# Kernel tuning notes

Hardware: AMD Instinct MI355X
Metric: run time of the kernel (lower is better)

## Reference

```python
import jax, jax.numpy as jnp
import numpy as np

N_NODES = 50000
N_EDGES = 800000
IN_FEATS = 64
H_FEATS = 128


def _uniform(key, shape, stdv):
    return jax.random.uniform(key, shape, jnp.float32, -stdv, stdv)


def setup_inputs() -> dict:
    key = jax.random.key(0)
    ks = jax.random.split(key, 16)
    inp = {}
    inp["features"] = jax.random.normal(ks[0], (N_NODES, IN_FEATS), jnp.float32)
    inp["mask"] = (jax.random.uniform(ks[1], (N_NODES, IN_FEATS)) > 0.3).astype(jnp.float32)
    inp["norm_g"] = jax.random.uniform(ks[2], (N_NODES, 1), jnp.float32, 0.05, 1.0)
    inp["norm_f"] = jax.random.uniform(ks[3], (N_NODES, 1), jnp.float32, 0.05, 1.0)
    inp["src_g"] = jax.random.randint(ks[4], (N_EDGES,), 0, N_NODES, jnp.int32)
    inp["dst_g"] = jax.random.randint(ks[5], (N_EDGES,), 0, N_NODES, jnp.int32)
    inp["src_f"] = jax.random.randint(ks[6], (N_EDGES,), 0, N_NODES, jnp.int32)
    inp["dst_f"] = jax.random.randint(ks[7], (N_EDGES,), 0, N_NODES, jnp.int32)
    # learned params, init per reset_parameters (uniform +/- 1/sqrt(out_feats))
    s1 = 1.0 / np.sqrt(H_FEATS)
    inp["W1"] = _uniform(ks[8], (IN_FEATS, H_FEATS), s1)
    inp["b1"] = _uniform(ks[9], (H_FEATS,), s1)
    s2 = 1.0 / np.sqrt(IN_FEATS)
    inp["wh"] = _uniform(ks[10], (H_FEATS, IN_FEATS), s2)
    inp["bh"] = _uniform(ks[11], (IN_FEATS,), s2)
    inp["ws"] = _uniform(ks[12], (IN_FEATS, IN_FEATS), s2)
    inp["bs"] = _uniform(ks[13], (IN_FEATS,), s2)
    return inp


def _aggregate(h, src, dst):
    # DGL update_all(copy_src, sum): gather source node feats per edge, sum at dst
    return jax.ops.segment_sum(h[src], dst, num_segments=N_NODES)


def reference(features, mask, norm_g, norm_f, src_g, dst_g, src_f, dst_f,
              W1, b1, wh, bh, ws, bs):
    x = features * mask                     # [N, in]
    # GCL (masked_gcn)
    h = (x @ W1) * norm_g                   # [N, h]
    h = _aggregate(h, src_g, dst_g) * norm_g + b1
    h = jax.nn.relu(h)
    # GCL_skip (output_gcn): h branch on g, skip branch s on f
    hb = (h @ wh) * norm_g                  # [N, in]
    sb = (x @ ws) * norm_f                  # [N, in]
    hb = _aggregate(hb, src_g, dst_g) * norm_g + bh
    sb = _aggregate(sb, src_f, dst_f) * norm_f + bs
    return jax.nn.sigmoid(hb + sb)
```

## Files before the change

kernel.cpp:

```cpp
#include <hip/hip_runtime.h>
#include <hip/hip_fp16.h>

#define N_NODES 50000
#define N_EDGES 800000
#define IN_F 64
#define H_F 128
#define NBUK 49
#define EPB 2048
#define NBLK 391

typedef unsigned short u16;
typedef unsigned int u32;

static __device__ __forceinline__ float4 ld4(const float* p) {
    return *reinterpret_cast<const float4*>(p);
}
static __device__ __forceinline__ void st4(float* p, float4 v) {
    *reinterpret_cast<float4*>(p) = v;
}
static __device__ __forceinline__ void st_h4(__half* p, float4 v) {
    union { __half h[4]; uint2 u; } pk;
    pk.h[0] = __float2half_rn(v.x);
    pk.h[1] = __float2half_rn(v.y);
    pk.h[2] = __float2half_rn(v.z);
    pk.h[3] = __float2half_rn(v.w);
    *reinterpret_cast<uint2*>(p) = pk.u;
}
static __device__ __forceinline__ void add_h4(float4& a, uint2 r) {
    __half2* p = reinterpret_cast<__half2*>(&r);
    float2 f0 = __half22float2(p[0]);
    float2 f1 = __half22float2(p[1]);
    a.x += f0.x; a.y += f0.y; a.z += f1.x; a.w += f1.y;
}

__global__ __launch_bounds__(256) void p1_count_k(
    const int* __restrict__ dst_g, const int* __restrict__ dst_f,
    int* __restrict__ cnt_g, int* __restrict__ cnt_f,
    const float* __restrict__ f, const float* __restrict__ m,
    const float* __restrict__ ng, __half* __restrict__ y)
{
    __shared__ int c[NBUK];
    const int tid = threadIdx.x;
    const int graph = blockIdx.x >= NBLK;
    const int blk = blockIdx.x - graph * NBLK;
    const int* dst = graph ? dst_f : dst_g;
    int* cnt = graph ? cnt_f : cnt_g;
    if (tid < NBUK) c[tid] = 0;
    __syncthreads();
    const int e0 = blk * EPB;
    const int e1 = min(e0 + EPB, N_EDGES);
    for (int e = e0 + tid; e < e1; e += 256) atomicAdd(&c[dst[e] >> 10], 1);
    __syncthreads();
    if (tid < NBUK) cnt[tid * NBLK + blk] = c[tid];
    for (int i = blockIdx.x * 256 + tid; i < N_NODES * (IN_F / 4);
         i += gridDim.x * 256) {
        int n = i >> 4;
        float s = ng[n];
        float4 a = ld4(f + 4 * i);
        float4 b = ld4(m + 4 * i);
        float4 r;
        r.x = a.x * b.x * s; r.y = a.y * b.y * s;
        r.z = a.z * b.z * s; r.w = a.w * b.w * s;
        st_h4(y + 4 * i, r);
    }
}

__global__ __launch_bounds__(1024) void s1_scan_k(
    const int* __restrict__ cnt_g, int* __restrict__ off_g, int* __restrict__ bb_g,
    const int* __restrict__ cnt_f, int* __restrict__ off_f, int* __restrict__ bb_f)
{
    __shared__ int part[1024];
    const int tid = threadIdx.x;
    const int TOT = NBUK * NBLK;
    const int chunk = (TOT + 1023) / 1024;
    for (int g = 0; g < 2; ++g) {
        const int* cnt = g ? cnt_f : cnt_g;
        int* off = g ? off_f : off_g;
        int* bb  = g ? bb_f  : bb_g;
        const int lo = tid * chunk;
        const int hi = min(lo + chunk, TOT);
        int s = 0;
        for (int i = lo; i < hi; ++i) s += cnt[i];
        part[tid] = s;
        __syncthreads();
        for (int o = 1; o < 1024; o <<= 1) {
            int v = (tid >= o) ? part[tid - o] : 0;
            __syncthreads();
            part[tid] += v;
            __syncthreads();
        }
        int ex = (tid == 0) ? 0 : part[tid - 1];
        for (int i = lo; i < hi; ++i) {
            off[i] = ex;
            if (i % NBLK == 0) bb[i / NBLK] = ex;
            ex += cnt[i];
        }
        if (tid == 0) bb[NBUK] = N_EDGES;
        __syncthreads();
    }
}

__global__ __launch_bounds__(256) void p2_part_k(
    const int* __restrict__ src_g, const int* __restrict__ dst_g,
    const int* __restrict__ off_g, u32* __restrict__ rec_g,
    const int* __restrict__ src_f, const int* __restrict__ dst_f,
    const int* __restrict__ off_f, u32* __restrict__ rec_f)
{
    __shared__ int base[NBUK];
    __shared__ int cur[NBUK];
    const int tid = threadIdx.x;
    const int graph = blockIdx.x >= NBLK;
    const int blk = blockIdx.x - graph * NBLK;
    const int* src = graph ? src_f : src_g;
    const int* dst = graph ? dst_f : dst_g;
    const int* off = graph ? off_f : off_g;
    u32* rec = graph ? rec_f : rec_g;
    if (tid < NBUK) { base[tid] = off[tid * NBLK + blk]; cur[tid] = 0; }
    __syncthreads();
    const int e0 = blk * EPB;
    const int e1 = min(e0 + EPB, N_EDGES);
    for (int e = e0 + tid; e < e1; e += 256) {
        int d = dst[e], s = src[e];
        int b = d >> 10;
        int p = atomicAdd(&cur[b], 1);
        rec[base[b] + p] = ((u32)s << 16) | (u32)d;
    }
}

__global__ __launch_bounds__(1024) void p3_build_k(
    const u32* __restrict__ rec_g, const int* __restrict__ bb_g,
    int* __restrict__ rp_g, u16* __restrict__ adj_g,
    const u32* __restrict__ rec_f, const int* __restrict__ bb_f,
    int* __restrict__ rp_f, u16* __restrict__ adj_f)
{
    __shared__ int hist[1024];
    __shared__ int tmp[1024];
    const int tid = threadIdx.x;
    const int graph = blockIdx.x >= NBUK;
    const int b = blockIdx.x - graph * NBUK;
    const u32* rec = graph ? rec_f : rec_g;
    const int* bb  = graph ? bb_f  : bb_g;
    int* rp  = graph ? rp_f : rp_g;
    u16* adj = graph ? adj_f : adj_g;
    const int e_base = bb[b];
    const int e_cnt  = bb[b + 1] - e_base;
    hist[tid] = 0;
    __syncthreads();
    for (int i = tid; i < e_cnt; i += 1024)
        atomicAdd(&hist[rec[e_base + i] & 1023], 1);
    __syncthreads();
    const int v = hist[tid];
    tmp[tid] = v;
    __syncthreads();
    for (int o = 1; o < 1024; o <<= 1) {
        int t = (tid >= o) ? tmp[tid - o] : 0;
        __syncthreads();
        tmp[tid] += t;
        __syncthreads();
    }
    const int excl = tmp[tid] - v;
    const int n = (b << 10) + tid;
    if (n < N_NODES) rp[n] = e_base + excl;
    if (b == NBUK - 1 && tid == 0) rp[N_NODES] = N_EDGES;
    hist[tid] = excl;
    __syncthreads();
    for (int i = tid; i < e_cnt; i += 1024) {
        u32 r = rec[e_base + i];
        int p = atomicAdd(&hist[r & 1023], 1);
        adj[e_base + p] = (u16)(r >> 16);
    }
}

static __device__ __forceinline__ float4 csr_row_sum_h4(
        const __half* __restrict__ tbl, const u16* __restrict__ adj,
        int e, int e1, int off) {
    float4 acc = make_float4(0.f, 0.f, 0.f, 0.f);
    for (; e + 4 <= e1; e += 4) {
        int s0 = adj[e], s1 = adj[e + 1], s2 = adj[e + 2], s3 = adj[e + 3];
        uint2 r0 = *reinterpret_cast<const uint2*>(tbl + (s0 << 6) + off);
        uint2 r1 = *reinterpret_cast<const uint2*>(tbl + (s1 << 6) + off);
        uint2 r2 = *reinterpret_cast<const uint2*>(tbl + (s2 << 6) + off);
        uint2 r3 = *reinterpret_cast<const uint2*>(tbl + (s3 << 6) + off);
        add_h4(acc, r0); add_h4(acc, r1); add_h4(acc, r2); add_h4(acc, r3);
    }
    for (; e < e1; ++e) {
        uint2 r = *reinterpret_cast<const uint2*>(tbl + (adj[e] << 6) + off);
        add_h4(acc, r);
    }
    return acc;
}

__global__ __launch_bounds__(256) void agg64_k(const __half* __restrict__ tbl,
        const int* __restrict__ rp, const u16* __restrict__ adj,
        float* __restrict__ out) {
    const int tid = threadIdx.x;
    const int fl = tid & 15;
    const int n  = blockIdx.x * 16 + (tid >> 4);
    if (n >= N_NODES) return;
    float4 acc = csr_row_sum_h4(tbl, adj, rp[n], rp[n + 1], fl << 2);
    st4(out + (n << 6) + (fl << 2), acc);
}

template<int K, int N, int SMODE, int EPI, int OUT16>
__global__ __launch_bounds__(256) void gemm_k(
    const float* __restrict__ A, const float* __restrict__ A2,
    const float* __restrict__ W, const float* __restrict__ rs,
    const float* __restrict__ bias, void* __restrict__ outv, int M)
{
    constexpr int CPT = N / 16;
    constexpr int AS  = K + 1;
    constexpr int KQ  = K / 4;
    __shared__ __align__(16) float Wl[K * N];
    __shared__ __align__(16) float Al[64 * AS];

    const int tid = threadIdx.x;
    const int n0  = blockIdx.x << 6;

    for (int i = tid; i < K * N / 4; i += 256) st4(&Wl[4 * i], ld4(W + 4 * i));
    for (int i4 = tid; i4 < 64 * KQ; i4 += 256) {
        int n  = i4 / KQ;
        int k4 = (i4 & (KQ - 1)) << 2;
        int gn = n0 + n;
        float4 v = make_float4(0.f, 0.f, 0.f, 0.f);
        if (gn < M) {
            v = ld4(A + gn * K + k4);
            if (SMODE == 1) {
                float4 m4 = ld4(A2 + gn * K + k4);
                v.x *= m4.x; v.y *= m4.y; v.z *= m4.z; v.w *= m4.w;
            }
        }
        float* p = &Al[n * AS + k4];
        p[0] = v.x; p[1] = v.y; p[2] = v.z; p[3] = v.w;
    }
    __syncthreads();

    const int tr = tid & 15;
    const int tc = tid >> 4;

    float acc[4][CPT];
#pragma unroll
    for (int i = 0; i < 4; ++i)
#pragma unroll
        for (int j = 0; j < CPT; ++j) acc[i][j] = 0.f;

#pragma unroll 4
    for (int k = 0; k < K; ++k) {
        float a0 = Al[(4 * tr + 0) * AS + k];
        float a1 = Al[(4 * tr + 1) * AS + k];
        float a2 = Al[(4 * tr + 2) * AS + k];
        float a3 = Al[(4 * tr + 3) * AS + k];
#pragma unroll
        for (int jq = 0; jq < CPT / 4; ++jq) {
            float4 w = ld4(&Wl[k * N + tc * CPT + 4 * jq]);
            acc[0][4 * jq + 0] += a0 * w.x; acc[0][4 * jq + 1] += a0 * w.y;
            acc[0][4 * jq + 2] += a0 * w.z; acc[0][4 * jq + 3] += a0 * w.w;
            acc[1][4 * jq + 0] += a1 * w.x; acc[1][4 * jq + 1] += a1 * w.y;
            acc[1][4 * jq + 2] += a1 * w.z; acc[1][4 * jq + 3] += a1 * w.w;
            acc[2][4 * jq + 0] += a2 * w.x; acc[2][4 * jq + 1] += a2 * w.y;
            acc[2][4 * jq + 2] += a2 * w.z; acc[2][4 * jq + 3] += a2 * w.w;
            acc[3][4 * jq + 0] += a3 * w.x; acc[3][4 * jq + 1] += a3 * w.y;
            acc[3][4 * jq + 2] += a3 * w.z; acc[3][4 * jq + 3] += a3 * w.w;
        }
    }

#pragma unroll
    for (int i = 0; i < 4; ++i) {
        int gn = n0 + 4 * tr + i;
        if (gn >= M) continue;
        float s = rs[gn];
#pragma unroll
        for (int jq = 0; jq < CPT / 4; ++jq) {
            float4 o;
            if (EPI == 1) {
                float4 b4 = ld4(bias + tc * CPT + 4 * jq);
                o.x = fmaxf(fmaf(acc[i][4 * jq + 0], s, b4.x), 0.f);
                o.y = fmaxf(fmaf(acc[i][4 * jq + 1], s, b4.y), 0.f);
                o.z = fmaxf(fmaf(acc[i][4 * jq + 2], s, b4.z), 0.f);
                o.w = fmaxf(fmaf(acc[i][4 * jq + 3], s, b4.w), 0.f);
            } else {
                o.x = acc[i][4 * jq + 0] * s; o.y = acc[i][4 * jq + 1] * s;
                o.z = acc[i][4 * jq + 2] * s; o.w = acc[i][4 * jq + 3] * s;
            }
            if (OUT16) {
                st_h4((__half*)outv + gn * N + tc * CPT + 4 * jq, o);
            } else {
                st4((float*)outv + gn * N + tc * CPT + 4 * jq, o);
            }
        }
    }
}

__global__ __launch_bounds__(256) void final2_k(
    const __half* __restrict__ hb, const __half* __restrict__ sb,
    const int* __restrict__ rp_g, const u16* __restrict__ adj_g,
    const int* __restrict__ rp_f, const u16* __restrict__ adj_f,
    const float* __restrict__ ng, const float* __restrict__ nf,
    const float* __restrict__ bh, const float* __restrict__ bs,
    float* __restrict__ out)
{
    const int tid = threadIdx.x;
    const int fl = tid & 15;
    const int n  = blockIdx.x * 16 + (tid >> 4);
    if (n >= N_NODES) return;
    const int off = fl << 2;
    float4 accg = csr_row_sum_h4(hb, adj_g, rp_g[n], rp_g[n + 1], off);
    float4 accf = csr_row_sum_h4(sb, adj_f, rp_f[n], rp_f[n + 1], off);
    const float g = ng[n], f = nf[n];
    float4 b4 = ld4(bh + off);
    float4 s4 = ld4(bs + off);
    float4 o;
    float t;
    t = accg.x * g + b4.x + accf.x * f + s4.x; o.x = 1.f / (1.f + expf(-t));
    t = accg.y * g + b4.y + accf.y * f + s4.y; o.y = 1.f / (1.f + expf(-t));
    t = accg.z * g + b4.z + accf.z * f + s4.z; o.z = 1.f / (1.f + expf(-t));
    t = accg.w * g + b4.w + accf.w * f + s4.w; o.w = 1.f / (1.f + expf(-t));
    st4(out + (n << 6) + off, o);
}

extern "C" void kernel_launch(void* const* d_in, const int* in_sizes, int n_in,
                              void* d_out, int out_size, void* d_ws, size_t ws_size,
                              hipStream_t stream) {
    const float* features = (const float*)d_in[0];
    const float* mask     = (const float*)d_in[1];
    const float* norm_g   = (const float*)d_in[2];
    const float* norm_f   = (const float*)d_in[3];
    const int*   src_g    = (const int*)d_in[4];
    const int*   dst_g    = (const int*)d_in[5];
    const int*   src_f    = (const int*)d_in[6];
    const int*   dst_f    = (const int*)d_in[7];
    const float* W1  = (const float*)d_in[8];
    const float* b1  = (const float*)d_in[9];
    const float* wh  = (const float*)d_in[10];
    const float* bh  = (const float*)d_in[11];
    const float* wsw = (const float*)d_in[12];
    const float* bs  = (const float*)d_in[13];
    float* out = (float*)d_out;
    float* ws  = (float*)d_ws;

    __half* y   = (__half*)ws;
    float*  z   = ws + 3200000;
    float*  t1  = ws + 6400000;
    __half* hb0 = (__half*)ws;
    __half* sb0 = (__half*)(ws + 3200000);
    int* creg  = (int*)(ws + 6400000);
    u32* rec_g = (u32*)creg;
    u32* rec_f = (u32*)(creg + 800000);
    int* cnt_g = creg + 1600000;
    int* cnt_f = creg + 1619159;
    int* off_g = creg + 1638318;
    int* off_f = creg + 1657477;
    int* pers  = (int*)(ws + 12800000);
    int* rp_g  = pers;
    int* rp_f  = pers + 50001;
    int* bb_g  = pers + 100002;
    int* bb_f  = pers + 100052;
    u16* adj_g = (u16*)(pers + 100102);
    u16* adj_f = (u16*)(pers + 500102);

    const int gblocks = (N_NODES + 63) / 64;
    const int nblk16  = (N_NODES + 15) / 16;

    p1_count_k<<<2 * NBLK, 256, 0, stream>>>(dst_g, dst_f, cnt_g, cnt_f,
                                             features, mask, norm_g, y);
    s1_scan_k<<<1, 1024, 0, stream>>>(cnt_g, off_g, bb_g, cnt_f, off_f, bb_f);
    p2_part_k<<<2 * NBLK, 256, 0, stream>>>(src_g, dst_g, off_g, rec_g,
                                            src_f, dst_f, off_f, rec_f);
    p3_build_k<<<2 * NBUK, 1024, 0, stream>>>(rec_g, bb_g, rp_g, adj_g,
                                              rec_f, bb_f, rp_f, adj_f);

    agg64_k<<<nblk16, 256, 0, stream>>>(y, rp_g, adj_g, z);

    gemm_k<64, 128, 0, 1, 0><<<gblocks, 256, 0, stream>>>(z, nullptr, W1, norm_g,
                                                          b1, (void*)t1, N_NODES);
    gemm_k<128, 64, 0, 2, 1><<<gblocks, 256, 0, stream>>>(t1, nullptr, wh, norm_g,
                                                          nullptr, (void*)hb0, N_NODES);
    gemm_k<64, 64, 1, 2, 1><<<gblocks, 256, 0, stream>>>(features, mask, wsw, norm_f,
                                                         nullptr, (void*)sb0, N_NODES);

    final2_k<<<nblk16, 256, 0, stream>>>(hb0, sb0, rp_g, adj_g, rp_f, adj_f,
                                         norm_g, norm_f, bh, bs, out);
}
```

Before: 294.2 us.

## Build CSR with fixed-capacity buckets via global atomics and widen gather loads

Merges the count, scan and partition passes into one kernel. Each block reserves space in fixed-capacity per-bucket regions through global atomic counters, so the single-block scan kernel and a second pass over the edges go away. Row starts and ends are now stored separately because buckets are no longer contiguous. The aggregation kernels switch to 8 lanes per node with 16-byte half-precision loads in place of 16 lanes with 8-byte loads. The risk is that edges are silently dropped if a bucket ever exceeds its capacity, which assumes a roughly uniform destination distribution.

```diff
diff --git a/kernel.cpp b/kernel.cpp
--- a/kernel.cpp
+++ b/kernel.cpp
@@ -8,6 +8,7 @@
 #define NBUK 49
 #define EPB 2048
 #define NBLK 391
+#define CAP 24576
 
 typedef unsigned short u16;
 typedef unsigned int u32;
@@ -26,32 +27,63 @@
     pk.h[3] = __float2half_rn(v.w);
     *reinterpret_cast<uint2*>(p) = pk.u;
 }
-static __device__ __forceinline__ void add_h4(float4& a, uint2 r) {
+static __device__ __forceinline__ void add_h8(float4& a, float4& b, uint4 r) {
     __half2* p = reinterpret_cast<__half2*>(&r);
     float2 f0 = __half22float2(p[0]);
     float2 f1 = __half22float2(p[1]);
+    float2 f2 = __half22float2(p[2]);
+    float2 f3 = __half22float2(p[3]);
     a.x += f0.x; a.y += f0.y; a.z += f1.x; a.w += f1.y;
-}
-
-__global__ __launch_bounds__(256) void p1_count_k(
-    const int* __restrict__ dst_g, const int* __restrict__ dst_f,
-    int* __restrict__ cnt_g, int* __restrict__ cnt_f,
+    b.x += f2.x; b.y += f2.y; b.z += f3.x; b.w += f3.y;
+}
+
+__global__ __launch_bounds__(256) void part_k(
+    const int* __restrict__ src_g, const int* __restrict__ dst_g, u32* __restrict__ rec_g,
+    const int* __restrict__ src_f, const int* __restrict__ dst_f, u32* __restrict__ rec_f,
+    int* __restrict__ bukcur,
     const float* __restrict__ f, const float* __restrict__ m,
     const float* __restrict__ ng, __half* __restrict__ y)
 {
     __shared__ int c[NBUK];
+    __shared__ int base[NBUK];
     const int tid = threadIdx.x;
     const int graph = blockIdx.x >= NBLK;
     const int blk = blockIdx.x - graph * NBLK;
+    const int* src = graph ? src_f : src_g;
     const int* dst = graph ? dst_f : dst_g;
-    int* cnt = graph ? cnt_f : cnt_g;
+    u32* rec = graph ? rec_f : rec_g;
+    int* cur = bukcur + graph * NBUK;
+
     if (tid < NBUK) c[tid] = 0;
     __syncthreads();
     const int e0 = blk * EPB;
     const int e1 = min(e0 + EPB, N_EDGES);
-    for (int e = e0 + tid; e < e1; e += 256) atomicAdd(&c[dst[e] >> 10], 1);
-    __syncthreads();
-    if (tid < NBUK) cnt[tid * NBLK + blk] = c[tid];
+
+    u32 r_[8];
+    bool v_[8];
+#pragma unroll
+    for (int j = 0; j < 8; ++j) {
+        int e = e0 + tid + j * 256;
+        v_[j] = (e < e1);
+        int d = 0, s = 0;
+        if (v_[j]) { d = dst[e]; s = src[e]; }
+        r_[j] = ((u32)s << 16) | (u32)d;
+        if (v_[j]) atomicAdd(&c[d >> 10], 1);
+    }
+    __syncthreads();
+    if (tid < NBUK) base[tid] = atomicAdd(&cur[tid], c[tid]);
+    __syncthreads();
+    if (tid < NBUK) c[tid] = 0;
+    __syncthreads();
+#pragma unroll
+    for (int j = 0; j < 8; ++j) {
+        if (v_[j]) {
+            u32 r = r_[j];
+            int b = (int)((r & 0xFFFFu) >> 10);
+            int p = base[b] + atomicAdd(&c[b], 1);
+            if (p < CAP) rec[b * CAP + p] = r;
+        }
+    }
     for (int i = blockIdx.x * 256 + tid; i < N_NODES * (IN_F / 4);
          i += gridDim.x * 256) {
         int n = i >> 4;
@@ -65,73 +97,12 @@
     }
 }
 
-__global__ __launch_bounds__(1024) void s1_scan_k(
-    const int* __restrict__ cnt_g, int* __restrict__ off_g, int* __restrict__ bb_g,
-    const int* __restrict__ cnt_f, int* __restrict__ off_f, int* __restrict__ bb_f)
-{
-    __shared__ int part[1024];
-    const int tid = threadIdx.x;
-    const int TOT = NBUK * NBLK;
-    const int chunk = (TOT + 1023) / 1024;
-    for (int g = 0; g < 2; ++g) {
-        const int* cnt = g ? cnt_f : cnt_g;
-        int* off = g ? off_f : off_g;
-        int* bb  = g ? bb_f  : bb_g;
-        const int lo = tid * chunk;
-        const int hi = min(lo + chunk, TOT);
-        int s = 0;
-        for (int i = lo; i < hi; ++i) s += cnt[i];
-        part[tid] = s;
-        __syncthreads();
-        for (int o = 1; o < 1024; o <<= 1) {
-            int v = (tid >= o) ? part[tid - o] : 0;
-            __syncthreads();
-            part[tid] += v;
-            __syncthreads();
-        }
-        int ex = (tid == 0) ? 0 : part[tid - 1];
-        for (int i = lo; i < hi; ++i) {
-            off[i] = ex;
-            if (i % NBLK == 0) bb[i / NBLK] = ex;
-            ex += cnt[i];
-        }
-        if (tid == 0) bb[NBUK] = N_EDGES;
-        __syncthreads();
-    }
-}
-
-__global__ __launch_bounds__(256) void p2_part_k(
-    const int* __restrict__ src_g, const int* __restrict__ dst_g,
-    const int* __restrict__ off_g, u32* __restrict__ rec_g,
-    const int* __restrict__ src_f, const int* __restrict__ dst_f,
-    const int* __restrict__ off_f, u32* __restrict__ rec_f)
-{
-    __shared__ int base[NBUK];
-    __shared__ int cur[NBUK];
-    const int tid = threadIdx.x;
-    const int graph = blockIdx.x >= NBLK;
-    const int blk = blockIdx.x - graph * NBLK;
-    const int* src = graph ? src_f : src_g;
-    const int* dst = graph ? dst_f : dst_g;
-    const int* off = graph ? off_f : off_g;
-    u32* rec = graph ? rec_f : rec_g;
-    if (tid < NBUK) { base[tid] = off[tid * NBLK + blk]; cur[tid] = 0; }
-    __syncthreads();
-    const int e0 = blk * EPB;
-    const int e1 = min(e0 + EPB, N_EDGES);
-    for (int e = e0 + tid; e < e1; e += 256) {
-        int d = dst[e], s = src[e];
-        int b = d >> 10;
-        int p = atomicAdd(&cur[b], 1);
-        rec[base[b] + p] = ((u32)s << 16) | (u32)d;
-    }
-}
-
 __global__ __launch_bounds__(1024) void p3_build_k(
-    const u32* __restrict__ rec_g, const int* __restrict__ bb_g,
-    int* __restrict__ rp_g, u16* __restrict__ adj_g,
-    const u32* __restrict__ rec_f, const int* __restrict__ bb_f,
-    int* __restrict__ rp_f, u16* __restrict__ adj_f)
+    const u32* __restrict__ rec_g, int* __restrict__ rps_g, int* __restrict__ rpe_g,
+    u16* __restrict__ adj_g,
+    const u32* __restrict__ rec_f, int* __restrict__ rps_f, int* __restrict__ rpe_f,
+    u16* __restrict__ adj_f,
+    const int* __restrict__ bukcur)
 {
     __shared__ int hist[1024];
     __shared__ int tmp[1024];
@@ -139,11 +110,12 @@
     const int graph = blockIdx.x >= NBUK;
     const int b = blockIdx.x - graph * NBUK;
     const u32* rec = graph ? rec_f : rec_g;
-    const int* bb  = graph ? bb_f  : bb_g;
-    int* rp  = graph ? rp_f : rp_g;
+    int* rps = graph ? rps_f : rps_g;
+    int* rpe = graph ? rpe_f : rpe_g;
     u16* adj = graph ? adj_f : adj_g;
-    const int e_base = bb[b];
-    const int e_cnt  = bb[b + 1] - e_base;
+    const int e_base = b * CAP;
+    const int e_cnt  = min(bukcur[graph * NBUK + b], CAP);
+
     hist[tid] = 0;
     __syncthreads();
     for (int i = tid; i < e_cnt; i += 1024)
@@ -158,10 +130,13 @@
         tmp[tid] += t;
         __syncthreads();
     }
-    const int excl = tmp[tid] - v;
+    const int incl = tmp[tid];
+    const int excl = incl - v;
     const int n = (b << 10) + tid;
-    if (n < N_NODES) rp[n] = e_base + excl;
-    if (b == NBUK - 1 && tid == 0) rp[N_NODES] = N_EDGES;
+    if (n < N_NODES) {
+        rps[n] = e_base + excl;
+        rpe[n] = e_base + incl;
+    }
     hist[tid] = excl;
     __syncthreads();
     for (int i = tid; i < e_cnt; i += 1024) {
@@ -171,34 +146,36 @@
     }
 }
 
-static __device__ __forceinline__ float4 csr_row_sum_h4(
+static __device__ __forceinline__ void csr_row_sum_h8(
         const __half* __restrict__ tbl, const u16* __restrict__ adj,
-        int e, int e1, int off) {
-    float4 acc = make_float4(0.f, 0.f, 0.f, 0.f);
+        int e, int e1, int off, float4& A, float4& B) {
     for (; e + 4 <= e1; e += 4) {
         int s0 = adj[e], s1 = adj[e + 1], s2 = adj[e + 2], s3 = adj[e + 3];
-        uint2 r0 = *reinterpret_cast<const uint2*>(tbl + (s0 << 6) + off);
-        uint2 r1 = *reinterpret_cast<const uint2*>(tbl + (s1 << 6) + off);
-        uint2 r2 = *reinterpret_cast<const uint2*>(tbl + (s2 << 6) + off);
-        uint2 r3 = *reinterpret_cast<const uint2*>(tbl + (s3 << 6) + off);
-        add_h4(acc, r0); add_h4(acc, r1); add_h4(acc, r2); add_h4(acc, r3);
+        uint4 r0 = *reinterpret_cast<const uint4*>(tbl + (s0 << 6) + off);
+        uint4 r1 = *reinterpret_cast<const uint4*>(tbl + (s1 << 6) + off);
+        uint4 r2 = *reinterpret_cast<const uint4*>(tbl + (s2 << 6) + off);
+        uint4 r3 = *reinterpret_cast<const uint4*>(tbl + (s3 << 6) + off);
+        add_h8(A, B, r0); add_h8(A, B, r1); add_h8(A, B, r2); add_h8(A, B, r3);
     }
     for (; e < e1; ++e) {
-        uint2 r = *reinterpret_cast<const uint2*>(tbl + (adj[e] << 6) + off);
-        add_h4(acc, r);
-    }
-    return acc;
+        uint4 r = *reinterpret_cast<const uint4*>(tbl + (adj[e] << 6) + off);
+        add_h8(A, B, r);
+    }
 }
 
 __global__ __launch_bounds__(256) void agg64_k(const __half* __restrict__ tbl,
-        const int* __restrict__ rp, const u16* __restrict__ adj,
-        float* __restrict__ out) {
-    const int tid = threadIdx.x;
-    const int fl = tid & 15;
-    const int n  = blockIdx.x * 16 + (tid >> 4);
+        const int* __restrict__ rps, const int* __restrict__ rpe,
+        const u16* __restrict__ adj, float* __restrict__ out) {
+    const int tid = threadIdx.x;
+    const int fl = tid & 7;
+    const int n  = blockIdx.x * 32 + (tid >> 3);
     if (n >= N_NODES) return;
-    float4 acc = csr_row_sum_h4(tbl, adj, rp[n], rp[n + 1], fl << 2);
-    st4(out + (n << 6) + (fl << 2), acc);
+    const int off = fl << 3;
+    float4 A = make_float4(0.f, 0.f, 0.f, 0.f);
+    float4 B = make_float4(0.f, 0.f, 0.f, 0.f);
+    csr_row_sum_h8(tbl, adj, rps[n], rpe[n], off, A, B);
+    st4(out + (n << 6) + off, A);
+    st4(out + (n << 6) + off + 4, B);
 }
 
 template<int K, int N, int SMODE, int EPI, int OUT16>
@@ -292,29 +269,40 @@
 
 __global__ __launch_bounds__(256) void final2_k(
     const __half* __restrict__ hb, const __half* __restrict__ sb,
-    const int* __restrict__ rp_g, const u16* __restrict__ adj_g,
-    const int* __restrict__ rp_f, const u16* __restrict__ adj_f,
+    const int* __restrict__ rps_g, const int* __restrict__ rpe_g,
+    const u16* __restrict__ adj_g,
+    const int* __restrict__ rps_f, const int* __restrict__ rpe_f,
+    const u16* __restrict__ adj_f,
     const float* __restrict__ ng, const float* __restrict__ nf,
     const float* __restrict__ bh, const float* __restrict__ bs,
     float* __restrict__ out)
 {
     const int tid = threadIdx.x;
-    const int fl = tid & 15;
-    const int n  = blockIdx.x * 16 + (tid >> 4);
+    const int fl = tid & 7;
+    const int n  = blockIdx.x * 32 + (tid >> 3);
     if (n >= N_NODES) return;
-    const int off = fl << 2;
-    float4 accg = csr_row_sum_h4(hb, adj_g, rp_g[n], rp_g[n + 1], off);
-    float4 accf = csr_row_sum_h4(sb, adj_f, rp_f[n], rp_f[n + 1], off);
+    const int off = fl << 3;
+    float4 Ag = make_float4(0.f, 0.f, 0.f, 0.f);
+    float4 Bg = make_float4(0.f, 0.f, 0.f, 0.f);
+    float4 Af = make_float4(0.f, 0.f, 0.f, 0.f);
+    float4 Bf = make_float4(0.f, 0.f, 0.f, 0.f);
+    csr_row_sum_h8(hb, adj_g, rps_g[n], rpe_g[n], off, Ag, Bg);
+    csr_row_sum_h8(sb, adj_f, rps_f[n], rpe_f[n], off, Af, Bf);
     const float g = ng[n], f = nf[n];
-    float4 b4 = ld4(bh + off);
-    float4 s4 = ld4(bs + off);
-    float4 o;
+    float4 b0 = ld4(bh + off), b1 = ld4(bh + off + 4);
+    float4 s0 = ld4(bs + off), s1 = ld4(bs + off + 4);
+    float4 o0, o1;
     float t;
-    t = accg.x * g + b4.x + accf.x * f + s4.x; o.x = 1.f / (1.f + expf(-t));
-    t = accg.y * g + b4.y + accf.y * f + s4.y; o.y = 1.f / (1.f + expf(-t));
-    t = accg.z * g + b4.z + accf.z * f + s4.z; o.z = 1.f / (1.f + expf(-t));
-    t = accg.w * g + b4.w + accf.w * f + s4.w; o.w = 1.f / (1.f + expf(-t));
-    st4(out + (n << 6) + off, o);
+    t = Ag.x * g + b0.x + Af.x * f + s0.x; o0.x = 1.f / (1.f + expf(-t));
+    t = Ag.y * g + b0.y + Af.y * f + s0.y; o0.y = 1.f / (1.f + expf(-t));
+    t = Ag.z * g + b0.z + Af.z * f + s0.z; o0.z = 1.f / (1.f + expf(-t));
+    t = Ag.w * g + b0.w + Af.w * f + s0.w; o0.w = 1.f / (1.f + expf(-t));
+    t = Bg.x * g + b1.x + Bf.x * f + s1.x; o1.x = 1.f / (1.f + expf(-t));
+    t = Bg.y * g + b1.y + Bf.y * f + s1.y; o1.y = 1.f / (1.f + expf(-t));
+    t = Bg.z * g + b1.z + Bf.z * f + s1.z; o1.z = 1.f / (1.f + expf(-t));
+    t = Bg.w * g + b1.w + Bf.w * f + s1.w; o1.w = 1.f / (1.f + expf(-t));
+    st4(out + (n << 6) + off, o0);
+    st4(out + (n << 6) + off + 4, o1);
 }
 
 extern "C" void kernel_launch(void* const* d_in, const int* in_sizes, int n_in,
@@ -342,33 +330,29 @@
     float*  t1  = ws + 6400000;
     __half* hb0 = (__half*)ws;
     __half* sb0 = (__half*)(ws + 3200000);
-    int* creg  = (int*)(ws + 6400000);
-    u32* rec_g = (u32*)creg;
-    u32* rec_f = (u32*)(creg + 800000);
-    int* cnt_g = creg + 1600000;
-    int* cnt_f = creg + 1619159;
-    int* off_g = creg + 1638318;
-    int* off_f = creg + 1657477;
-    int* pers  = (int*)(ws + 12800000);
-    int* rp_g  = pers;
-    int* rp_f  = pers + 50001;
-    int* bb_g  = pers + 100002;
-    int* bb_f  = pers + 100052;
-    u16* adj_g = (u16*)(pers + 100102);
-    u16* adj_f = (u16*)(pers + 500102);
+    int* creg   = (int*)(ws + 6400000);
+    u32* rec_g  = (u32*)creg;
+    u32* rec_f  = (u32*)(creg + NBUK * CAP);
+    int* bukcur = creg + 2 * NBUK * CAP;
+    int* pers   = (int*)(ws + 12800000);
+    int* rps_g  = pers;
+    int* rpe_g  = pers + 50000;
+    int* rps_f  = pers + 100000;
+    int* rpe_f  = pers + 150000;
+    u16* adj_g  = (u16*)(pers + 200000);
+    u16* adj_f  = adj_g + NBUK * CAP;
 
     const int gblocks = (N_NODES + 63) / 64;
-    const int nblk16  = (N_NODES + 15) / 16;
-
-    p1_count_k<<<2 * NBLK, 256, 0, stream>>>(dst_g, dst_f, cnt_g, cnt_f,
-                                             features, mask, norm_g, y);
-    s1_scan_k<<<1, 1024, 0, stream>>>(cnt_g, off_g, bb_g, cnt_f, off_f, bb_f);
-    p2_part_k<<<2 * NBLK, 256, 0, stream>>>(src_g, dst_g, off_g, rec_g,
-                                            src_f, dst_f, off_f, rec_f);
-    p3_build_k<<<2 * NBUK, 1024, 0, stream>>>(rec_g, bb_g, rp_g, adj_g,
-                                              rec_f, bb_f, rp_f, adj_f);
-
-    agg64_k<<<nblk16, 256, 0, stream>>>(y, rp_g, adj_g, z);
+    const int nblk32  = (N_NODES + 31) / 32;
+
+    hipMemsetAsync(bukcur, 0, 2 * NBUK * sizeof(int), stream);
+    part_k<<<2 * NBLK, 256, 0, stream>>>(src_g, dst_g, rec_g,
+                                         src_f, dst_f, rec_f, bukcur,
+                                         features, mask, norm_g, y);
+    p3_build_k<<<2 * NBUK, 1024, 0, stream>>>(rec_g, rps_g, rpe_g, adj_g,
+                                              rec_f, rps_f, rpe_f, adj_f, bukcur);
+
+    agg64_k<<<nblk32, 256, 0, stream>>>(y, rps_g, rpe_g, adj_g, z);
 
     gemm_k<64, 128, 0, 1, 0><<<gblocks, 256, 0, stream>>>(z, nullptr, W1, norm_g,
                                                           b1, (void*)t1, N_NODES);
@@ -377,6 +361,7 @@
     gemm_k<64, 64, 1, 2, 1><<<gblocks, 256, 0, stream>>>(features, mask, wsw, norm_f,
                                                          nullptr, (void*)sb0, N_NODES);
 
-    final2_k<<<nblk16, 256, 0, stream>>>(hb0, sb0, rp_g, adj_g, rp_f, adj_f,
+    final2_k<<<nblk32, 256, 0, stream>>>(hb0, sb0, rps_g, rpe_g, adj_g,
+                                         rps_f, rpe_f, adj_f,
                                          norm_g, norm_f, bh, bs, out);
 }
```

Result: faster. 247.5 us (-15.9%).
